# Optimization experiments

Measured on AMD Instinct MI355X. Metric: run time of the kernel, lower is better.

## Reference

```python
import jax, jax.numpy as jnp
import numpy as np

B, T, I, H, O = 128, 1024, 64, 512, 64
NOISE_STD = 0.05
DT = 0.5
G = 0.9


def setup_inputs() -> dict:
    key = jax.random.key(0)
    k_in, k_wi, k_wrec, k_wo, k_noise = jax.random.split(key, 5)
    inp = jax.random.normal(k_in, (B, T, I), dtype=jnp.float32)
    wi = jax.random.normal(k_wi, (I, H), dtype=jnp.float32)  # std=1 init
    wrec = jax.random.normal(k_wrec, (H, H), dtype=jnp.float32) * (G / np.sqrt(H))
    wo = jax.random.normal(k_wo, (H, O), dtype=jnp.float32) * (1.0 / H)
    brec = jnp.zeros((H,), dtype=jnp.float32)
    h0 = jnp.zeros((H,), dtype=jnp.float32)
    noise = jax.random.normal(k_noise, (B, T, H), dtype=jnp.float32)
    return {"input": inp, "wi": wi, "wrec": wrec, "wo": wo,
            "brec": brec, "h0": h0, "noise": noise}


def reference(input, wi, wrec, wo, brec, h0, noise):
    dt = jnp.float32(DT)
    noise_scale = jnp.float32(np.sqrt(DT) * NOISE_STD)
    # Precompute input projection + bias for all timesteps: [B,T,H]
    xw = jnp.einsum('bti,ih->bth', input, wi) + brec
    h_init = jnp.broadcast_to(h0, (input.shape[0], h0.shape[0]))

    def step(h, inputs_t):
        xw_t, n_t = inputs_t  # [B,H] each
        rec = jnp.tanh(h) @ wrec.T + xw_t
        h_new = (1.0 - dt) * h + dt * rec + noise_scale * n_t
        out_t = jnp.tanh(h_new) @ wo  # readout nonlinearity defaults to tanh
        return h_new, out_t

    # scan over time: move T to leading axis
    _, outs = jax.lax.scan(step, h_init,
                           (jnp.swapaxes(xw, 0, 1), jnp.swapaxes(noise, 0, 1)))
    return jnp.swapaxes(outs, 0, 1)  # [B,T,O]
```

## Files before the change

### kernel.cpp

```cpp
#include <hip/hip_runtime.h>


#define TSTEPS 1024
#define HDIM   512
#define IDIM   64
#define ODIM   64
#define NSCALE 0.035355339059327376f

typedef short bf16x8  __attribute__((ext_vector_type(8)));
typedef float f32x4   __attribute__((ext_vector_type(4)));
typedef int   int4v   __attribute__((ext_vector_type(4)));
typedef int   int2v   __attribute__((ext_vector_type(2)));
typedef short short4v __attribute__((ext_vector_type(4)));

__device__ __forceinline__ unsigned short f2bf(float f){
  unsigned u = __float_as_uint(f);
  u = (u + 0x7fffu + ((u >> 16) & 1u)) >> 16;
  return (unsigned short)u;
}
__device__ __forceinline__ float tanh_fast(float x){
  float e = __expf(2.0f * x);
  return 1.0f - 2.0f / (e + 1.0f);
}

template<int OFF>
__device__ __forceinline__ int4v g_load16(const char* p){
  int4v r;
  asm volatile("global_load_dwordx4 %0, %1, off offset:%2 sc0 sc1"
               : "=v"(r) : "v"(p), "n"(OFF) : "memory");
  return r;
}
__device__ __forceinline__ void g_store8(void* p, int2v v){
  asm volatile("global_store_dwordx2 %0, %1, off sc0 sc1" :: "v"(p), "v"(v) : "memory");
}
__device__ __forceinline__ void g_store4(void* p, unsigned v){
  asm volatile("global_store_dword %0, %1, off sc0 sc1" :: "v"(p), "v"(v) : "memory");
}

__global__ void prep_kernel(const float* __restrict__ wi, const float* __restrict__ wrec,
                            const float* __restrict__ wo,
                            unsigned short* __restrict__ wrecb,
                            unsigned short* __restrict__ wiT,
                            unsigned short* __restrict__ woT){
  int i = blockIdx.x * 256 + threadIdx.x;
  if (i < HDIM*HDIM){
    wrecb[i] = f2bf(wrec[i]);
  } else if (i < HDIM*HDIM + HDIM*IDIM){
    int q = i - HDIM*HDIM; int j = q >> 6, ii = q & 63;
    wiT[q] = f2bf(wi[ii*HDIM + j]);
  } else if (i < HDIM*HDIM + HDIM*IDIM + ODIM*HDIM){
    int q = i - HDIM*HDIM - HDIM*IDIM; int o = q >> 9, k = q & 511;
    woT[q] = f2bf(wo[k*ODIM + o]);
  }
}

__global__ __launch_bounds__(320, 1) void rnn_scan(
    const float* __restrict__ input, const float* __restrict__ noise,
    const float* __restrict__ brec,  const float* __restrict__ h0,
    const unsigned short* __restrict__ wrecb,
    const unsigned short* __restrict__ wiT,
    const unsigned short* __restrict__ woT,
    unsigned short* __restrict__ tanhbuf,
    unsigned int*  __restrict__ flags,
    float* __restrict__ out)
{
  __shared__ __align__(16) short in_tile[2][1024];
  __shared__ float lds_ro[2][4][256];
  __shared__ volatile int mbox[2];

  const int tid = threadIdx.x;
  const int bid = blockIdx.x;
  const int g   = bid & 7;
  const int s   = bid >> 3;
  const int l   = tid & 63;
  const int w   = tid >> 6;

  if (tid == 0){ mbox[0] = 0; mbox[1] = 0; }

  char* const slot0 = (char*)tanhbuf + (0*8 + g)*16384;
  char* const slot1 = (char*)tanhbuf + (1*8 + g)*16384;
  unsigned int* const gflags = flags + g*64;

  if (w < 4){
    const int lr = l & 15, kg = l >> 4;
    const int b0 = g * 16;
    const int jrow = s*64 + w*16 + lr;

    bf16x8 Arec[16];
#pragma unroll
    for (int kt = 0; kt < 16; ++kt)
      Arec[kt] = *(const bf16x8*)(wrecb + jrow*HDIM + kt*32 + kg*8);
    bf16x8 Awi[2];
#pragma unroll
    for (int u = 0; u < 2; ++u)
      Awi[u] = *(const bf16x8*)(wiT + jrow*IDIM + u*32 + kg*8);
    bf16x8 Awo[4];
    if (s < 4){
      const int ocol = s*16 + lr;
#pragma unroll
      for (int u = 0; u < 4; ++u)
        Awo[u] = *(const bf16x8*)(woT + ocol*HDIM + (w*4 + u)*32 + kg*8);
    }

    const int j0 = s*64 + w*16 + 4*kg;
    const f32x4 brec4 = *(const f32x4*)(brec + j0);
    const f32x4 h04   = *(const f32x4*)(h0 + j0);
    float h[4] = {h04[0], h04[1], h04[2], h04[3]};

    const float* nbase = noise + ((long)(b0 + lr))*TSTEPS*HDIM + j0;
    const int pub_off = s*2048 + (w>>1)*1024
                      + (lr + 16*((w&1)*2 + (kg>>1)))*16 + (kg&1)*8;

    const f32x4 zero4 = {0.f, 0.f, 0.f, 0.f};

    auto stage_input = [&](int tt, int bufi){
      int m = tid >> 4, i0 = (tid & 15) * 4;
      const float* src = input + ((long)(b0 + m) * TSTEPS + tt) * IDIM + i0;
      float4 v = *(const float4*)src;
      short4v pk;
      pk.x = (short)f2bf(v.x); pk.y = (short)f2bf(v.y);
      pk.z = (short)f2bf(v.z); pk.w = (short)f2bf(v.w);
      int byt = (m*128 + i0*2) ^ ((m & 7) << 4);
      *(short4v*)((char*)in_tile[bufi] + byt) = pk;
    };
    auto xw_mfma = [&](int bufi) -> f32x4 {
      f32x4 a = zero4;
#pragma unroll
      for (int u = 0; u < 2; ++u){
        int byt = (lr*128 + u*64 + kg*16) ^ ((lr & 7) << 4);
        bf16x8 bfv = *(const bf16x8*)((const char*)in_tile[bufi] + byt);
        a = __builtin_amdgcn_mfma_f32_16x16x32_bf16(Awi[u], bfv, a, 0, 0, 0);
      }
      return a;
    };
    auto publish = [&](char* slq, float t0, float t1, float t2, float t3){
      int2v v;
      v.x = (int)((unsigned)f2bf(t0) | ((unsigned)f2bf(t1) << 16));
      v.y = (int)((unsigned)f2bf(t2) | ((unsigned)f2bf(t3) << 16));
      g_store8(slq + pub_off, v);
    };

    f32x4 nz4 = *(const f32x4*)nbase;
    publish(slot0, tanh_fast(h04[0]), tanh_fast(h04[1]),
                   tanh_fast(h04[2]), tanh_fast(h04[3]));
    asm volatile("s_waitcnt vmcnt(0)" ::: "memory");
    if (l == 0) g_store4(gflags + (s*4 + w), 1u);
    stage_input(0, 0);
    __syncthreads();
    f32x4 acc_xw = xw_mfma(0);

    for (int t = 0; t <= TSTEPS; ++t){
      const bool compute = (t < TSTEPS);
      const int p = t & 1;
      const char* slp = p ? slot1 : slot0;

      while (mbox[p] < t + 1) {}

      const char* gb0 = slp + l*16;
      const char* gb1 = gb0 + 4096;
      const char* gb2 = gb0 + 8192;
      const char* gb3 = gb0 + 12288;
      int4v g0  = g_load16<0>(gb0),  g1  = g_load16<1024>(gb0),
            g2  = g_load16<2048>(gb0), g3 = g_load16<3072>(gb0);
      int4v g4  = g_load16<0>(gb1),  g5  = g_load16<1024>(gb1),
            g6  = g_load16<2048>(gb1), g7 = g_load16<3072>(gb1);
      int4v g8  = g_load16<0>(gb2),  g9  = g_load16<1024>(gb2),
            g10 = g_load16<2048>(gb2), g11 = g_load16<3072>(gb2);
      int4v g12 = g_load16<0>(gb3),  g13 = g_load16<1024>(gb3),
            g14 = g_load16<2048>(gb3), g15 = g_load16<3072>(gb3);
      asm volatile("s_waitcnt vmcnt(0)" ::: "memory");
      __builtin_amdgcn_sched_barrier(0);

      if (compute){
        f32x4 a0 = acc_xw, a1 = zero4, a2 = zero4, a3 = zero4;
#define MF(gv, kt, ac) ac = __builtin_amdgcn_mfma_f32_16x16x32_bf16(Arec[kt], __builtin_bit_cast(bf16x8, gv), ac, 0, 0, 0)
        MF(g0,0,a0);   MF(g1,1,a1);   MF(g2,2,a2);   MF(g3,3,a3);
        MF(g4,4,a0);   MF(g5,5,a1);   MF(g6,6,a2);   MF(g7,7,a3);
        MF(g8,8,a0);   MF(g9,9,a1);   MF(g10,10,a2); MF(g11,11,a3);
        MF(g12,12,a0); MF(g13,13,a1); MF(g14,14,a2); MF(g15,15,a3);
#undef MF
        float tb[4];
#pragma unroll
        for (int r = 0; r < 4; ++r){
          float rec = a0[r] + a1[r] + a2[r] + a3[r] + brec4[r];
          float hn  = 0.5f*h[r] + 0.5f*rec + NSCALE*nz4[r];
          h[r] = hn;
          tb[r] = tanh_fast(hn);
        }
        publish(p ? slot0 : slot1, tb[0], tb[1], tb[2], tb[3]);
        asm volatile("s_waitcnt vmcnt(0)" ::: "memory");
        if (l == 0) g_store4(gflags + ((t+1)&1)*32 + s*4 + w, (unsigned)(t + 2));
        if (t + 1 < TSTEPS)
          nz4 = *(const f32x4*)(nbase + (long)(t + 1) * HDIM);
      }

      if (t >= 1 && s < 4){
        f32x4 ro = zero4;
#define RO(gv, u) ro = __builtin_amdgcn_mfma_f32_16x16x32_bf16(Awo[u], __builtin_bit_cast(bf16x8, gv), ro, 0, 0, 0)
        if (w == 0){ RO(g0,0);  RO(g1,1);  RO(g2,2);  RO(g3,3); }
        else if (w == 1){ RO(g4,0);  RO(g5,1);  RO(g6,2);  RO(g7,3); }
        else if (w == 2){ RO(g8,0);  RO(g9,1);  RO(g10,2); RO(g11,3); }
        else            { RO(g12,0); RO(g13,1); RO(g14,2); RO(g15,3); }
#undef RO
#pragma unroll
        for (int r = 0; r < 4; ++r)
          lds_ro[t & 1][w][(4*kg + r)*16 + lr] = ro[r];
      }
      if (t + 1 < TSTEPS) stage_input(t + 1, (t + 1) & 1);
      __syncthreads();
      if (t >= 1 && s < 4){
        const int idx = (tid & 15)*16 + (tid >> 4);
        float v = lds_ro[t & 1][0][idx] + lds_ro[t & 1][1][idx]
                + lds_ro[t & 1][2][idx] + lds_ro[t & 1][3][idx];
        out[(((long)(b0 + (tid >> 4)))*TSTEPS + (t - 1))*ODIM + s*16 + (tid & 15)] = v;
      }
      if (t + 1 < TSTEPS) acc_xw = xw_mfma((t + 1) & 1);
    }
  } else {
    auto pollto = [&](int q, int tgt){
      const unsigned int* fp = gflags + q*32 + (l & 31);
      for (;;){
        unsigned a;
        asm volatile("global_load_dword %0, %1, off sc0 sc1\n\t"
                     "s_waitcnt vmcnt(0)"
                     : "=v"(a) : "v"(fp) : "memory");
        int m = (int)a;
#pragma unroll
        for (int d = 1; d < 32; d <<= 1){
          int o = __shfl_xor(m, d); m = (o < m) ? o : m;
        }
        if (m >= tgt){ if (l == 0) mbox[q] = m; break; }
      }
    };
    __syncthreads();
    pollto(0, 1);
    for (int t = 0; t <= TSTEPS; ++t){
      if (t < TSTEPS) pollto((t + 1) & 1, t + 2);
      __syncthreads();
    }
  }
}

extern "C" void kernel_launch(void* const* d_in, const int* in_sizes, int n_in,
                              void* d_out, int out_size, void* d_ws, size_t ws_size,
                              hipStream_t stream){
  (void)in_sizes; (void)n_in; (void)ws_size; (void)out_size;
  const float* input = (const float*)d_in[0];
  const float* wi    = (const float*)d_in[1];
  const float* wrec  = (const float*)d_in[2];
  const float* wo    = (const float*)d_in[3];
  const float* brec  = (const float*)d_in[4];
  const float* h0    = (const float*)d_in[5];
  const float* noise = (const float*)d_in[6];
  float* out = (float*)d_out;

  char* ws = (char*)d_ws;
  unsigned short* wrecb = (unsigned short*)(ws);
  unsigned short* wiT   = (unsigned short*)(ws + 524288);
  unsigned short* woT   = (unsigned short*)(ws + 589824);
  unsigned short* tanhb = (unsigned short*)(ws + 655360);
  unsigned int*   flags = (unsigned int*)  (ws + 917504);

  hipMemsetAsync(ws + 917504, 0, 2048, stream);
  prep_kernel<<<1280, 256, 0, stream>>>(wi, wrec, wo, wrecb, wiT, woT);
  rnn_scan<<<64, 320, 0, stream>>>(input, noise, brec, h0, wrecb, wiT, woT,
                                   tanhb, flags, out);
}
```

Measured before the change: 2.912 ms.

## Replace flag-based cross-block sync with sentinel-polled data slots

Drops the flag array, the dedicated polling wave and the per-step __syncthreads. Consumers now spin directly on the published tanh data in a 4-slot ring, re-loading only chunks that still hold a sentinel value, and producers clear the slot two steps ahead. The readout is computed per wave over the full hidden dimension, so the LDS reduction goes away, and the input projection is loaded straight from global memory rather than staged in LDS. This cuts a flag store/poll round trip and block barriers from the critical path. The cost is redundant readout MFMAs, a larger workspace memset, and correctness that depends on the sentinel never matching a real packed bf16 pair.

```diff
diff --git a/kernel.cpp b/kernel.cpp
--- a/kernel.cpp
+++ b/kernel.cpp
@@ -6,12 +6,12 @@
 #define IDIM   64
 #define ODIM   64
 #define NSCALE 0.035355339059327376f
+#define SENTI  ((int)0x7F7F7F7F)
 
 typedef short bf16x8  __attribute__((ext_vector_type(8)));
 typedef float f32x4   __attribute__((ext_vector_type(4)));
 typedef int   int4v   __attribute__((ext_vector_type(4)));
 typedef int   int2v   __attribute__((ext_vector_type(2)));
-typedef short short4v __attribute__((ext_vector_type(4)));
 
 __device__ __forceinline__ unsigned short f2bf(float f){
   unsigned u = __float_as_uint(f);
@@ -22,20 +22,12 @@
   float e = __expf(2.0f * x);
   return 1.0f - 2.0f / (e + 1.0f);
 }
-
-template<int OFF>
-__device__ __forceinline__ int4v g_load16(const char* p){
-  int4v r;
-  asm volatile("global_load_dwordx4 %0, %1, off offset:%2 sc0 sc1"
-               : "=v"(r) : "v"(p), "n"(OFF) : "memory");
-  return r;
-}
 __device__ __forceinline__ void g_store8(void* p, int2v v){
   asm volatile("global_store_dwordx2 %0, %1, off sc0 sc1" :: "v"(p), "v"(v) : "memory");
 }
-__device__ __forceinline__ void g_store4(void* p, unsigned v){
-  asm volatile("global_store_dword %0, %1, off sc0 sc1" :: "v"(p), "v"(v) : "memory");
-}
+#define GLD(dst, base, IMM) \
+  asm volatile("global_load_dwordx4 %0, %1, off offset:" #IMM " sc0 sc1" \
+               : "=v"(dst) : "v"(base) : "memory")
 
 __global__ void prep_kernel(const float* __restrict__ wi, const float* __restrict__ wrec,
                             const float* __restrict__ wo,
@@ -54,189 +46,165 @@
   }
 }
 
-__global__ __launch_bounds__(320, 1) void rnn_scan(
+__global__ __launch_bounds__(256, 1) void rnn_scan(
     const float* __restrict__ input, const float* __restrict__ noise,
     const float* __restrict__ brec,  const float* __restrict__ h0,
     const unsigned short* __restrict__ wrecb,
     const unsigned short* __restrict__ wiT,
     const unsigned short* __restrict__ woT,
     unsigned short* __restrict__ tanhbuf,
-    unsigned int*  __restrict__ flags,
     float* __restrict__ out)
 {
-  __shared__ __align__(16) short in_tile[2][1024];
-  __shared__ float lds_ro[2][4][256];
-  __shared__ volatile int mbox[2];
-
-  const int tid = threadIdx.x;
-  const int bid = blockIdx.x;
-  const int g   = bid & 7;
-  const int s   = bid >> 3;
-  const int l   = tid & 63;
-  const int w   = tid >> 6;
-
-  if (tid == 0){ mbox[0] = 0; mbox[1] = 0; }
-
-  char* const slot0 = (char*)tanhbuf + (0*8 + g)*16384;
-  char* const slot1 = (char*)tanhbuf + (1*8 + g)*16384;
-  unsigned int* const gflags = flags + g*64;
-
-  if (w < 4){
-    const int lr = l & 15, kg = l >> 4;
-    const int b0 = g * 16;
-    const int jrow = s*64 + w*16 + lr;
-
-    bf16x8 Arec[16];
+  const int tid = threadIdx.x, bid = blockIdx.x;
+  const int g = bid & 7, s = bid >> 3;
+  const int l = tid & 63, w = tid >> 6;
+  const int lr = l & 15, kg = l >> 4;
+  const int b0 = g * 16;
+  const int jrow = s*64 + w*16 + lr;
+
+  bf16x8 Arec[16];
 #pragma unroll
-    for (int kt = 0; kt < 16; ++kt)
-      Arec[kt] = *(const bf16x8*)(wrecb + jrow*HDIM + kt*32 + kg*8);
-    bf16x8 Awi[2];
+  for (int kt = 0; kt < 16; ++kt)
+    Arec[kt] = *(const bf16x8*)(wrecb + jrow*HDIM + kt*32 + kg*8);
+  bf16x8 Awi0 = *(const bf16x8*)(wiT + jrow*IDIM +  0 + kg*8);
+  bf16x8 Awi1 = *(const bf16x8*)(wiT + jrow*IDIM + 32 + kg*8);
+  const bool ro_on = (s < 4);
+  bf16x8 Awo[16] = {};
+  if (ro_on){
+    const int ocol = s*16 + lr;
 #pragma unroll
-    for (int u = 0; u < 2; ++u)
-      Awi[u] = *(const bf16x8*)(wiT + jrow*IDIM + u*32 + kg*8);
-    bf16x8 Awo[4];
-    if (s < 4){
-      const int ocol = s*16 + lr;
+    for (int ci = 0; ci < 16; ++ci)
+      Awo[ci] = *(const bf16x8*)(woT + ocol*HDIM + ci*32 + kg*8);
+  }
+
+  const int j0 = s*64 + w*16 + 4*kg;
+  const f32x4 brec4 = *(const f32x4*)(brec + j0);
+  const f32x4 h04   = *(const f32x4*)(h0 + j0);
+  float h[4] = {h04[0], h04[1], h04[2], h04[3]};
+  const float* nbase = noise + ((long)(b0 + lr))*TSTEPS*HDIM + j0;
+  const float* irow  = input + ((long)(b0 + lr))*TSTEPS*IDIM;
+
+  const int pub_off = s*2048 + (w>>1)*1024
+                    + (lr + 16*((w&1)*2 + (kg>>1)))*16 + (kg&1)*8;
+  char* const tbb = (char*)tanhbuf;
+  const f32x4 zero4 = {0.f, 0.f, 0.f, 0.f};
+
+  auto pack8 = [&](float4 a, float4 b) -> bf16x8 {
+    bf16x8 r;
+    r[0]=(short)f2bf(a.x); r[1]=(short)f2bf(a.y); r[2]=(short)f2bf(a.z); r[3]=(short)f2bf(a.w);
+    r[4]=(short)f2bf(b.x); r[5]=(short)f2bf(b.y); r[6]=(short)f2bf(b.z); r[7]=(short)f2bf(b.w);
+    return r;
+  };
+
+  {
+    int2v v;
+    v.x = (int)((unsigned)f2bf(tanh_fast(h04[0])) | ((unsigned)f2bf(tanh_fast(h04[1])) << 16));
+    v.y = (int)((unsigned)f2bf(tanh_fast(h04[2])) | ((unsigned)f2bf(tanh_fast(h04[3])) << 16));
+    g_store8(tbb + g*16384 + pub_off, v);
+  }
+  int4v g0,g1,g2,g3,g4,g5,g6,g7,g8,g9,g10,g11,g12,g13,g14,g15;
+  {
+    const char* gb0 = tbb + g*16384 + l*16;
+    const char* gb1 = gb0+4096; const char* gb2 = gb0+8192; const char* gb3 = gb0+12288;
+    GLD(g0,gb0,0); GLD(g1,gb0,1024); GLD(g2,gb0,2048); GLD(g3,gb0,3072);
+    GLD(g4,gb1,0); GLD(g5,gb1,1024); GLD(g6,gb1,2048); GLD(g7,gb1,3072);
+    GLD(g8,gb2,0); GLD(g9,gb2,1024); GLD(g10,gb2,2048); GLD(g11,gb2,3072);
+    GLD(g12,gb3,0); GLD(g13,gb3,1024); GLD(g14,gb3,2048); GLD(g15,gb3,3072);
+  }
+  f32x4 nz4 = *(const f32x4*)nbase;
+  f32x4 acc_xw;
+  {
+    const float* ip = irow;
+    float4 fa = *(const float4*)(ip + 8*kg),      fb = *(const float4*)(ip + 8*kg + 4);
+    float4 fc = *(const float4*)(ip + 32 + 8*kg), fd = *(const float4*)(ip + 32 + 8*kg + 4);
+    acc_xw = __builtin_amdgcn_mfma_f32_16x16x32_bf16(Awi0, pack8(fa,fb), zero4, 0,0,0);
+    acc_xw = __builtin_amdgcn_mfma_f32_16x16x32_bf16(Awi1, pack8(fc,fd), acc_xw, 0,0,0);
+  }
+
+  unsigned pend = 0xFFFFu;
+  const int TLAST = ro_on ? TSTEPS : TSTEPS - 1;
+
+  for (int t = 0; t <= TLAST; ++t){
+    {
+      const char* gb0 = tbb + ((t&3)*8 + g)*16384 + l*16;
+      const char* gb1 = gb0+4096; const char* gb2 = gb0+8192; const char* gb3 = gb0+12288;
+      for (;;){
+        asm volatile("s_waitcnt vmcnt(0)" ::: "memory");
+        __builtin_amdgcn_sched_barrier(0);
+        unsigned np = 0;
+#define CHKC(J, GV) if (pend & (1u<<J)){ \
+          int bad = (GV[0]==SENTI)|(GV[1]==SENTI)|(GV[2]==SENTI)|(GV[3]==SENTI); \
+          if (__any(bad)) np |= (1u<<J); }
+        CHKC(0,g0)  CHKC(1,g1)  CHKC(2,g2)  CHKC(3,g3)
+        CHKC(4,g4)  CHKC(5,g5)  CHKC(6,g6)  CHKC(7,g7)
+        CHKC(8,g8)  CHKC(9,g9)  CHKC(10,g10) CHKC(11,g11)
+        CHKC(12,g12) CHKC(13,g13) CHKC(14,g14) CHKC(15,g15)
+#undef CHKC
+        if (!np) break;
+#define RLD(J, GV, B, IMM) if (np & (1u<<J)) GLD(GV, B, IMM);
+        RLD(0,g0,gb0,0) RLD(1,g1,gb0,1024) RLD(2,g2,gb0,2048) RLD(3,g3,gb0,3072)
+        RLD(4,g4,gb1,0) RLD(5,g5,gb1,1024) RLD(6,g6,gb1,2048) RLD(7,g7,gb1,3072)
+        RLD(8,g8,gb2,0) RLD(9,g9,gb2,1024) RLD(10,g10,gb2,2048) RLD(11,g11,gb2,3072)
+        RLD(12,g12,gb3,0) RLD(13,g13,gb3,1024) RLD(14,g14,gb3,2048) RLD(15,g15,gb3,3072)
+#undef RLD
+        pend = np;
+      }
+    }
+    __builtin_amdgcn_sched_barrier(0);
+
+    if (t < TSTEPS){
+      f32x4 a0 = acc_xw, a1 = zero4, a2 = zero4, a3 = zero4;
+#define MF(GV, KT, AC) AC = __builtin_amdgcn_mfma_f32_16x16x32_bf16(Arec[KT], __builtin_bit_cast(bf16x8, GV), AC, 0, 0, 0)
+      MF(g0,0,a0);   MF(g1,1,a1);   MF(g2,2,a2);   MF(g3,3,a3);
+      MF(g4,4,a0);   MF(g5,5,a1);   MF(g6,6,a2);   MF(g7,7,a3);
+      MF(g8,8,a0);   MF(g9,9,a1);   MF(g10,10,a2); MF(g11,11,a3);
+      MF(g12,12,a0); MF(g13,13,a1); MF(g14,14,a2); MF(g15,15,a3);
+#undef MF
+      float tb[4];
 #pragma unroll
-      for (int u = 0; u < 4; ++u)
-        Awo[u] = *(const bf16x8*)(woT + ocol*HDIM + (w*4 + u)*32 + kg*8);
-    }
-
-    const int j0 = s*64 + w*16 + 4*kg;
-    const f32x4 brec4 = *(const f32x4*)(brec + j0);
-    const f32x4 h04   = *(const f32x4*)(h0 + j0);
-    float h[4] = {h04[0], h04[1], h04[2], h04[3]};
-
-    const float* nbase = noise + ((long)(b0 + lr))*TSTEPS*HDIM + j0;
-    const int pub_off = s*2048 + (w>>1)*1024
-                      + (lr + 16*((w&1)*2 + (kg>>1)))*16 + (kg&1)*8;
-
-    const f32x4 zero4 = {0.f, 0.f, 0.f, 0.f};
-
-    auto stage_input = [&](int tt, int bufi){
-      int m = tid >> 4, i0 = (tid & 15) * 4;
-      const float* src = input + ((long)(b0 + m) * TSTEPS + tt) * IDIM + i0;
-      float4 v = *(const float4*)src;
-      short4v pk;
-      pk.x = (short)f2bf(v.x); pk.y = (short)f2bf(v.y);
-      pk.z = (short)f2bf(v.z); pk.w = (short)f2bf(v.w);
-      int byt = (m*128 + i0*2) ^ ((m & 7) << 4);
-      *(short4v*)((char*)in_tile[bufi] + byt) = pk;
-    };
-    auto xw_mfma = [&](int bufi) -> f32x4 {
-      f32x4 a = zero4;
-#pragma unroll
-      for (int u = 0; u < 2; ++u){
-        int byt = (lr*128 + u*64 + kg*16) ^ ((lr & 7) << 4);
-        bf16x8 bfv = *(const bf16x8*)((const char*)in_tile[bufi] + byt);
-        a = __builtin_amdgcn_mfma_f32_16x16x32_bf16(Awi[u], bfv, a, 0, 0, 0);
+      for (int r = 0; r < 4; ++r){
+        float rec = a0[r] + a1[r] + a2[r] + a3[r] + brec4[r];
+        float hn  = 0.5f*h[r] + 0.5f*rec + NSCALE*nz4[r];
+        h[r] = hn;
+        tb[r] = tanh_fast(hn);
       }
-      return a;
-    };
-    auto publish = [&](char* slq, float t0, float t1, float t2, float t3){
-      int2v v;
-      v.x = (int)((unsigned)f2bf(t0) | ((unsigned)f2bf(t1) << 16));
-      v.y = (int)((unsigned)f2bf(t2) | ((unsigned)f2bf(t3) << 16));
-      g_store8(slq + pub_off, v);
-    };
-
-    f32x4 nz4 = *(const f32x4*)nbase;
-    publish(slot0, tanh_fast(h04[0]), tanh_fast(h04[1]),
-                   tanh_fast(h04[2]), tanh_fast(h04[3]));
-    asm volatile("s_waitcnt vmcnt(0)" ::: "memory");
-    if (l == 0) g_store4(gflags + (s*4 + w), 1u);
-    stage_input(0, 0);
-    __syncthreads();
-    f32x4 acc_xw = xw_mfma(0);
-
-    for (int t = 0; t <= TSTEPS; ++t){
-      const bool compute = (t < TSTEPS);
-      const int p = t & 1;
-      const char* slp = p ? slot1 : slot0;
-
-      while (mbox[p] < t + 1) {}
-
-      const char* gb0 = slp + l*16;
-      const char* gb1 = gb0 + 4096;
-      const char* gb2 = gb0 + 8192;
-      const char* gb3 = gb0 + 12288;
-      int4v g0  = g_load16<0>(gb0),  g1  = g_load16<1024>(gb0),
-            g2  = g_load16<2048>(gb0), g3 = g_load16<3072>(gb0);
-      int4v g4  = g_load16<0>(gb1),  g5  = g_load16<1024>(gb1),
-            g6  = g_load16<2048>(gb1), g7 = g_load16<3072>(gb1);
-      int4v g8  = g_load16<0>(gb2),  g9  = g_load16<1024>(gb2),
-            g10 = g_load16<2048>(gb2), g11 = g_load16<3072>(gb2);
-      int4v g12 = g_load16<0>(gb3),  g13 = g_load16<1024>(gb3),
-            g14 = g_load16<2048>(gb3), g15 = g_load16<3072>(gb3);
-      asm volatile("s_waitcnt vmcnt(0)" ::: "memory");
-      __builtin_amdgcn_sched_barrier(0);
-
-      if (compute){
-        f32x4 a0 = acc_xw, a1 = zero4, a2 = zero4, a3 = zero4;
-#define MF(gv, kt, ac) ac = __builtin_amdgcn_mfma_f32_16x16x32_bf16(Arec[kt], __builtin_bit_cast(bf16x8, gv), ac, 0, 0, 0)
-        MF(g0,0,a0);   MF(g1,1,a1);   MF(g2,2,a2);   MF(g3,3,a3);
-        MF(g4,4,a0);   MF(g5,5,a1);   MF(g6,6,a2);   MF(g7,7,a3);
-        MF(g8,8,a0);   MF(g9,9,a1);   MF(g10,10,a2); MF(g11,11,a3);
-        MF(g12,12,a0); MF(g13,13,a1); MF(g14,14,a2); MF(g15,15,a3);
-#undef MF
-        float tb[4];
-#pragma unroll
-        for (int r = 0; r < 4; ++r){
-          float rec = a0[r] + a1[r] + a2[r] + a3[r] + brec4[r];
-          float hn  = 0.5f*h[r] + 0.5f*rec + NSCALE*nz4[r];
-          h[r] = hn;
-          tb[r] = tanh_fast(hn);
-        }
-        publish(p ? slot0 : slot1, tb[0], tb[1], tb[2], tb[3]);
-        asm volatile("s_waitcnt vmcnt(0)" ::: "memory");
-        if (l == 0) g_store4(gflags + ((t+1)&1)*32 + s*4 + w, (unsigned)(t + 2));
-        if (t + 1 < TSTEPS)
-          nz4 = *(const f32x4*)(nbase + (long)(t + 1) * HDIM);
-      }
-
-      if (t >= 1 && s < 4){
-        f32x4 ro = zero4;
-#define RO(gv, u) ro = __builtin_amdgcn_mfma_f32_16x16x32_bf16(Awo[u], __builtin_bit_cast(bf16x8, gv), ro, 0, 0, 0)
-        if (w == 0){ RO(g0,0);  RO(g1,1);  RO(g2,2);  RO(g3,3); }
-        else if (w == 1){ RO(g4,0);  RO(g5,1);  RO(g6,2);  RO(g7,3); }
-        else if (w == 2){ RO(g8,0);  RO(g9,1);  RO(g10,2); RO(g11,3); }
-        else            { RO(g12,0); RO(g13,1); RO(g14,2); RO(g15,3); }
-#undef RO
-#pragma unroll
-        for (int r = 0; r < 4; ++r)
-          lds_ro[t & 1][w][(4*kg + r)*16 + lr] = ro[r];
-      }
-      if (t + 1 < TSTEPS) stage_input(t + 1, (t + 1) & 1);
-      __syncthreads();
-      if (t >= 1 && s < 4){
-        const int idx = (tid & 15)*16 + (tid >> 4);
-        float v = lds_ro[t & 1][0][idx] + lds_ro[t & 1][1][idx]
-                + lds_ro[t & 1][2][idx] + lds_ro[t & 1][3][idx];
-        out[(((long)(b0 + (tid >> 4)))*TSTEPS + (t - 1))*ODIM + s*16 + (tid & 15)] = v;
-      }
-      if (t + 1 < TSTEPS) acc_xw = xw_mfma((t + 1) & 1);
-    }
-  } else {
-    auto pollto = [&](int q, int tgt){
-      const unsigned int* fp = gflags + q*32 + (l & 31);
-      for (;;){
-        unsigned a;
-        asm volatile("global_load_dword %0, %1, off sc0 sc1\n\t"
-                     "s_waitcnt vmcnt(0)"
-                     : "=v"(a) : "v"(fp) : "memory");
-        int m = (int)a;
-#pragma unroll
-        for (int d = 1; d < 32; d <<= 1){
-          int o = __shfl_xor(m, d); m = (o < m) ? o : m;
-        }
-        if (m >= tgt){ if (l == 0) mbox[q] = m; break; }
-      }
-    };
-    __syncthreads();
-    pollto(0, 1);
-    for (int t = 0; t <= TSTEPS; ++t){
-      if (t < TSTEPS) pollto((t + 1) & 1, t + 2);
-      __syncthreads();
+      int2v pv;
+      pv.x = (int)((unsigned)f2bf(tb[0]) | ((unsigned)f2bf(tb[1]) << 16));
+      pv.y = (int)((unsigned)f2bf(tb[2]) | ((unsigned)f2bf(tb[3]) << 16));
+      g_store8(tbb + (((t+1)&3)*8 + g)*16384 + pub_off, pv);
+      int2v sv; sv.x = SENTI; sv.y = SENTI;
+      g_store8(tbb + (((t+3)&3)*8 + g)*16384 + pub_off, sv);
+    }
+
+    if (t >= 1 && ro_on){
+      f32x4 ro = zero4;
+#define ROX(GV, CI) ro = __builtin_amdgcn_mfma_f32_16x16x32_bf16(Awo[CI], __builtin_bit_cast(bf16x8, GV), ro, 0, 0, 0)
+      ROX(g0,0);   ROX(g1,1);   ROX(g2,2);   ROX(g3,3);
+      ROX(g4,4);   ROX(g5,5);   ROX(g6,6);   ROX(g7,7);
+      ROX(g8,8);   ROX(g9,9);   ROX(g10,10); ROX(g11,11);
+      ROX(g12,12); ROX(g13,13); ROX(g14,14); ROX(g15,15);
+#undef ROX
+      if ((lr >> 2) == w)
+        *(f32x4*)(out + (((long)(b0 + lr))*TSTEPS + (t - 1))*ODIM + s*16 + 4*kg) = ro;
+    }
+
+    if (t < TLAST){
+      const char* gb0 = tbb + (((t+1)&3)*8 + g)*16384 + l*16;
+      const char* gb1 = gb0+4096; const char* gb2 = gb0+8192; const char* gb3 = gb0+12288;
+      GLD(g0,gb0,0); GLD(g1,gb0,1024); GLD(g2,gb0,2048); GLD(g3,gb0,3072);
+      GLD(g4,gb1,0); GLD(g5,gb1,1024); GLD(g6,gb1,2048); GLD(g7,gb1,3072);
+      GLD(g8,gb2,0); GLD(g9,gb2,1024); GLD(g10,gb2,2048); GLD(g11,gb2,3072);
+      GLD(g12,gb3,0); GLD(g13,gb3,1024); GLD(g14,gb3,2048); GLD(g15,gb3,3072);
+      pend = 0xFFFFu;
+    }
+
+    if (t + 1 < TSTEPS){
+      nz4 = *(const f32x4*)(nbase + (long)(t + 1) * HDIM);
+      const float* ip = irow + (t + 1) * IDIM;
+      float4 fa = *(const float4*)(ip + 8*kg),      fb = *(const float4*)(ip + 8*kg + 4);
+      float4 fc = *(const float4*)(ip + 32 + 8*kg), fd = *(const float4*)(ip + 32 + 8*kg + 4);
+      acc_xw = __builtin_amdgcn_mfma_f32_16x16x32_bf16(Awi0, pack8(fa,fb), zero4, 0,0,0);
+      acc_xw = __builtin_amdgcn_mfma_f32_16x16x32_bf16(Awi1, pack8(fc,fd), acc_xw, 0,0,0);
     }
   }
 }
@@ -259,10 +227,8 @@
   unsigned short* wiT   = (unsigned short*)(ws + 524288);
   unsigned short* woT   = (unsigned short*)(ws + 589824);
   unsigned short* tanhb = (unsigned short*)(ws + 655360);
-  unsigned int*   flags = (unsigned int*)  (ws + 917504);
-
-  hipMemsetAsync(ws + 917504, 0, 2048, stream);
+
+  hipMemsetAsync(ws + 655360, 0x7F, 524288, stream);
   prep_kernel<<<1280, 256, 0, stream>>>(wi, wrec, wo, wrecb, wiT, woT);
-  rnn_scan<<<64, 320, 0, stream>>>(input, noise, brec, h0, wrecb, wiT, woT,
-                                   tanhb, flags, out);
-}
+  rnn_scan<<<64, 256, 0, stream>>>(input, noise, brec, h0, wrecb, wiT, woT, tanhb, out);
+}
```

New measurement: 4.114 ms. 41.3% more time.
